# Kernel optimization log

Measured on AMD Instinct MI355X. Metric: run time of the kernel, lower is better.

Reference implementation:

```python
import jax, jax.numpy as jnp
import numpy as np

N_FQK, N_FV, N_REL, N_VAL, N_KNOW = 512, 256, 128, 64, 256
TOPK_QK, TOPK_V, TOPK_REL, TOPK_VAL = 64, 32, 16, 3
FQK_END = N_FQK
FV_END = N_FQK + N_FV
REL_END = FV_END + N_REL
VAL_END = REL_END + N_VAL
TOTAL = VAL_END + N_KNOW


def setup_inputs() -> dict:
    key = jax.random.key(0)
    k1, k2, k3, k4, k5 = jax.random.split(key, 5)
    B, S, D, DS = 8, 4096, 1024, 64
    x = jax.random.normal(k1, (B, S, D), dtype=jnp.float32)
    importance = jax.random.uniform(k2, (B, S), dtype=jnp.float32)
    proj_w = jax.random.normal(k3, (DS, D), dtype=jnp.float32) * (1.0 / np.sqrt(D))
    proj_b = jax.random.normal(k4, (DS,), dtype=jnp.float32) * 0.01
    neuron_emb = jax.random.normal(k5, (TOTAL, DS), dtype=jnp.float32) * 0.02
    return {"x": x, "importance": importance, "proj_w": proj_w,
            "proj_b": proj_b, "neuron_emb": neuron_emb}


def _topk_sparsify(w, k):
    # keep top-k values per row, zero elsewhere
    vals, idx = jax.lax.top_k(w, k)
    B = w.shape[0]
    sparse = jnp.zeros_like(w).at[jnp.arange(B)[:, None], idx].set(vals)
    return sparse, idx


def reference(x, importance, proj_w, proj_b, neuron_emb):
    # shared projection + normalized neuron embeddings (eval: dropout off,
    # no excitability bonus)
    h = jnp.einsum('bsd,kd->bsk', x, proj_w) + proj_b          # [B,S,d_space]
    emb_n = neuron_emb / jnp.linalg.norm(neuron_emb, axis=-1, keepdims=True)
    all_logits = jnp.einsum('bsk,nk->bsn', h, emb_n)            # [B,S,TOTAL]

    def agg(logits):
        pref = jax.nn.softmax(logits, axis=-1)                  # [B,S,n]
        return jnp.einsum('bs,bsn->bn', importance, pref)

    w_qk = agg(all_logits[..., :FQK_END])
    _, idx_qk = jax.lax.top_k(w_qk, TOPK_QK)
    idx_qk = jnp.sort(idx_qk, axis=-1)

    w_v = agg(all_logits[..., FQK_END:FV_END])
    _, idx_v = jax.lax.top_k(w_v, TOPK_V)
    idx_v = jnp.sort(idx_v, axis=-1)

    rel_logits = all_logits[..., FV_END:REL_END]
    # relational_Q and relational_K use the same logits slice (eval mode)
    rel_dense_Q = agg(rel_logits)
    rel_dense_K = agg(rel_logits)
    rel_Q, _ = _topk_sparsify(rel_dense_Q, TOPK_REL)
    rel_K, _ = _topk_sparsify(rel_dense_K, TOPK_REL)

    val_dense = agg(all_logits[..., REL_END:VAL_END])
    val_w, _ = _topk_sparsify(val_dense, TOPK_VAL)

    return idx_qk, idx_v, rel_Q, rel_K, val_w
```

## Files before the change

### kernel.cpp

```cpp
#include <hip/hip_runtime.h>


typedef short short8 __attribute__((ext_vector_type(8)));
typedef float f32x4 __attribute__((ext_vector_type(4)));
typedef unsigned int uint4v __attribute__((ext_vector_type(4)));

__device__ __forceinline__ unsigned short f32_to_bf16(float f) {
  unsigned u = __float_as_uint(f);
  u += 0x7FFF + ((u >> 16) & 1);
  return (unsigned short)(u >> 16);
}
__device__ __forceinline__ float bf16_to_f32(unsigned short h) {
  return __uint_as_float(((unsigned)h) << 16);
}

__device__ __forceinline__ unsigned cvt_pk_bf16(float a, float b) {
  unsigned r;
  asm("v_cvt_pk_bf16_f32 %0, %1, %2" : "=v"(r) : "v"(a), "v"(b));
  return r;
}

__device__ __forceinline__ void split8v(const f32x4& v0, const f32x4& v1,
                                        short8& hi, short8& lo) {
  unsigned hp[4], lp[4];
#pragma unroll
  for (int j = 0; j < 4; ++j) {
    float a = (j < 2) ? v0[2 * j] : v1[2 * j - 4];
    float b = (j < 2) ? v0[2 * j + 1] : v1[2 * j - 3];
    unsigned p = cvt_pk_bf16(a, b);
    float ra = a - __uint_as_float(p << 16);
    float rb = b - __uint_as_float(p & 0xFFFF0000u);
    hp[j] = p;
    lp[j] = cvt_pk_bf16(ra, rb);
  }
  hi = __builtin_bit_cast(short8, (uint4v){hp[0], hp[1], hp[2], hp[3]});
  lo = __builtin_bit_cast(short8, (uint4v){lp[0], lp[1], lp[2], lp[3]});
}

#define MFMA(a, b, c) __builtin_amdgcn_mfma_f32_16x16x32_bf16(a, b, c, 0, 0, 0)
#define WAITVM(n) asm volatile("s_waitcnt vmcnt(" #n ")" ::: "memory")

typedef const __attribute__((address_space(1))) unsigned int guint;
typedef __attribute__((address_space(3))) unsigned int luint;
__device__ __forceinline__ void stage16(const float* g, float* l) {
  __builtin_amdgcn_global_load_lds((guint*)g, (luint*)l, 16, 0, 0);
}
__device__ __forceinline__ void bar() {
  asm volatile("" ::: "memory");
  __builtin_amdgcn_s_barrier();
  asm volatile("" ::: "memory");
}

__global__ __launch_bounds__(256) void k_prep(const float* __restrict__ pw,
                                              const float* __restrict__ emb,
                                              unsigned short* __restrict__ whi,
                                              unsigned short* __restrict__ wlo,
                                              unsigned short* __restrict__ ehi,
                                              unsigned short* __restrict__ elo) {
  int tid = blockIdx.x * 256 + threadIdx.x;
  for (int i = tid; i < 65536; i += gridDim.x * 256) {
    float v = pw[i];
    unsigned short h = f32_to_bf16(v);
    whi[i] = h;
    wlo[i] = f32_to_bf16(v - bf16_to_f32(h));
  }
  int wid = tid >> 6, lane = tid & 63;
  int nw = gridDim.x * 4;
  for (int n = wid; n < 960; n += nw) {
    float v = emb[n * 64 + lane];
    float s = v * v;
#pragma unroll
    for (int off = 1; off < 64; off <<= 1) s += __shfl_xor(s, off);
    float vn = v / sqrtf(s);
    unsigned short h = f32_to_bf16(vn);
    ehi[n * 64 + lane] = h;
    elo[n * 64 + lane] = f32_to_bf16(vn - bf16_to_f32(h));
  }
}

__global__ __launch_bounds__(256, 4) void k_main(
    const float* __restrict__ x, const unsigned short* __restrict__ whi,
    const unsigned short* __restrict__ wlo, const float* __restrict__ pb,
    const unsigned short* __restrict__ ehi, const unsigned short* __restrict__ elo,
    const float* __restrict__ imp, float* __restrict__ pp) {
  __shared__ __align__(16) float xt[5][32][32];
  __shared__ __align__(16) unsigned short hxh[32][64];
  __shared__ __align__(16) unsigned short hxl[32][64];
  __shared__ float zpart[4][32][4];
  __shared__ float coefL[32][4];

  const int tid = threadIdx.x, w = tid >> 6, lane = tid & 63;
  const int q = lane >> 4, c = lane & 15;
  const int row0 = blockIdx.x * 32;
  const int nt0 = w;

  const int srow = tid >> 3;
  const int scol = ((tid & 7) ^ (srow & 7)) * 4;
  const float* sbase = x + (size_t)(row0 + srow) * 1024 + scol;
  auto STAGEX = [&](int slot, int ks) {
    stage16(sbase + ks * 32, &xt[slot][0][0] + (w << 8));
  };

  const unsigned short* bwh = whi + (size_t)(nt0 * 16 + c) * 1024 + q * 8;
  const unsigned short* bwl = wlo + (size_t)(nt0 * 16 + c) * 1024 + q * 8;

  f32x4 acc0 = {0.f, 0.f, 0.f, 0.f}, acc1 = {0.f, 0.f, 0.f, 0.f};

  const unsigned sw = (unsigned)((c & 7) << 4);
  const unsigned off1 = ((unsigned)(q * 32)) ^ sw;
  const unsigned off2 = ((unsigned)(q * 32 + 16)) ^ sw;
  const char* xby = (const char*)&xt[0][0][0] + (size_t)c * 128;

  int rs = 0, wsl = 4;
  auto projstep = [&](short8 B_hi, short8 B_lo) {
    const char* bp = xby + rs * 4096;
    f32x4 a0 = *(const f32x4*)(bp + off1);
    f32x4 a1 = *(const f32x4*)(bp + off2);
    f32x4 a2 = *(const f32x4*)(bp + 2048 + off1);
    f32x4 a3 = *(const f32x4*)(bp + 2048 + off2);
    short8 ah, al;
    split8v(a0, a1, ah, al);
    acc0 = MFMA(ah, B_hi, acc0);
    acc0 = MFMA(ah, B_lo, acc0);
    acc0 = MFMA(al, B_hi, acc0);
    split8v(a2, a3, ah, al);
    acc1 = MFMA(ah, B_hi, acc1);
    acc1 = MFMA(ah, B_lo, acc1);
    acc1 = MFMA(al, B_hi, acc1);
    ++rs; if (rs == 5) rs = 0;
  };
  auto loadB = [&](short8 (&h)[2], short8 (&l)[2], int g) {
    h[0] = *(const short8*)(bwh + (2 * g) * 32);
    h[1] = *(const short8*)(bwh + (2 * g + 1) * 32);
    l[0] = *(const short8*)(bwl + (2 * g) * 32);
    l[1] = *(const short8*)(bwl + (2 * g + 1) * 32);
  };

  short8 BhA[2], BlA[2], BhB[2], BlB[2];
  loadB(BhA, BlA, 0);
  STAGEX(0, 0); STAGEX(1, 1); STAGEX(2, 2); STAGEX(3, 3);

  auto gpair = [&](int g) {
    loadB(BhB, BlB, g + 1);
    WAITVM(6); bar();
    STAGEX(wsl, 2 * g + 4); ++wsl; if (wsl == 5) wsl = 0;
    projstep(BhA[0], BlA[0]);
    WAITVM(7); bar();
    STAGEX(wsl, 2 * g + 5); ++wsl; if (wsl == 5) wsl = 0;
    projstep(BhA[1], BlA[1]);
    loadB(BhA, BlA, g + 2);
    WAITVM(6); bar();
    STAGEX(wsl, 2 * g + 6); ++wsl; if (wsl == 5) wsl = 0;
    projstep(BhB[0], BlB[0]);
    WAITVM(7); bar();
    STAGEX(wsl, 2 * g + 7); ++wsl; if (wsl == 5) wsl = 0;
    projstep(BhB[1], BlB[1]);
  };
  gpair(0); gpair(2); gpair(4); gpair(6); gpair(8); gpair(10); gpair(12);
  loadB(BhB, BlB, 15);
  WAITVM(7); bar(); projstep(BhA[0], BlA[0]);
  WAITVM(6); bar(); projstep(BhA[1], BlA[1]);
  WAITVM(1); bar(); projstep(BhB[0], BlB[0]);
  WAITVM(0); bar(); projstep(BhB[1], BlB[1]);

  float bias = pb[nt0 * 16 + c];
#pragma unroll
  for (int mt = 0; mt < 2; ++mt) {
    f32x4 a = mt ? acc1 : acc0;
#pragma unroll
    for (int r = 0; r < 4; ++r) {
      float val = a[r] + bias;
      int row = mt * 16 + q * 4 + r;
      unsigned colb = (unsigned)((nt0 * 16 + c) * 2);
      unsigned o = (unsigned)(row * 128) + (colb ^ ((unsigned)(row & 7) << 4));
      unsigned short h = f32_to_bf16(val);
      *(unsigned short*)((char*)&hxh[0][0] + o) = h;
      *(unsigned short*)((char*)&hxl[0][0] + o) = f32_to_bf16(val - bf16_to_f32(h));
    }
  }
  __syncthreads();

  short8 Ahi[2][2], Alo[2][2];
#pragma unroll
  for (int mt = 0; mt < 2; ++mt) {
    int row = mt * 16 + c;
    unsigned rsw = (unsigned)((row & 7) << 4);
#pragma unroll
    for (int k2 = 0; k2 < 2; ++k2) {
      unsigned o = (unsigned)(row * 128) + (((unsigned)(k2 * 64 + q * 16)) ^ rsw);
      Ahi[mt][k2] = *(const short8*)((const char*)&hxh[0][0] + o);
      Alo[mt][k2] = *(const short8*)((const char*)&hxl[0][0] + o);
    }
  }

  const size_t ebq = (size_t)c * 64 + q * 8;
  short8 eA[4], eB[4];
  auto LOADE = [&](short8 (&d)[4], int i) {
    size_t eb = (size_t)(w + 4 * i) * 1024 + ebq;
    d[0] = *(const short8*)(ehi + eb);
    d[1] = *(const short8*)(ehi + eb + 32);
    d[2] = *(const short8*)(elo + eb);
    d[3] = *(const short8*)(elo + eb + 32);
  };

  f32x4 zacc0 = {0.f, 0.f, 0.f, 0.f}, zacc1 = {0.f, 0.f, 0.f, 0.f};
  auto zflush = [&](int seg) {
#pragma unroll
    for (int mt = 0; mt < 2; ++mt)
#pragma unroll
      for (int r = 0; r < 4; ++r) {
        float v = mt ? zacc1[r] : zacc0[r];
        v += __shfl_xor(v, 1); v += __shfl_xor(v, 2);
        v += __shfl_xor(v, 4); v += __shfl_xor(v, 8);
        if (c == 0) zpart[w][mt * 16 + q * 4 + r][seg] = v;
      }
    zacc0 = (f32x4){0.f, 0.f, 0.f, 0.f};
    zacc1 = (f32x4){0.f, 0.f, 0.f, 0.f};
  };

  int cur_seg = 0;
  auto step1 = [&](int i, short8 (&e)[4]) {
    int nt = w + 4 * i;
    int s = (nt < 32) ? 0 : (nt < 48) ? 1 : (nt < 56) ? 2 : 3;
    if (s != cur_seg) { zflush(cur_seg); cur_seg = s; }
#pragma unroll
    for (int mt = 0; mt < 2; ++mt) {
      f32x4 l = {0.f, 0.f, 0.f, 0.f};
      l = MFMA(Ahi[mt][0], e[0], l); l = MFMA(Ahi[mt][1], e[1], l);
      l = MFMA(Ahi[mt][0], e[2], l); l = MFMA(Ahi[mt][1], e[3], l);
      l = MFMA(Alo[mt][0], e[0], l); l = MFMA(Alo[mt][1], e[1], l);
#pragma unroll
      for (int r = 0; r < 4; ++r) {
        if (mt == 0) zacc0[r] += __expf(l[r]); else zacc1[r] += __expf(l[r]);
      }
    }
  };
  LOADE(eA, 0);
#pragma unroll
  for (int j = 0; j < 7; ++j) {
    LOADE(eB, 2 * j + 1); step1(2 * j, eA);
    LOADE(eA, 2 * j + 2); step1(2 * j + 1, eB);
  }
  step1(14, eA);
  zflush(cur_seg);
  __syncthreads();
  if (tid < 128) {
    int row = tid & 31, sg = tid >> 5;
    float Z = zpart[0][row][sg] + zpart[1][row][sg] + zpart[2][row][sg] + zpart[3][row][sg];
    coefL[row][sg] = imp[row0 + row] / Z;
  }
  __syncthreads();

  float* ppb = pp + (size_t)blockIdx.x * 960;
  f32x4 cf0, cf1;
  int cs2 = -1;
  auto step2 = [&](int i, short8 (&e)[4]) {
    int nt = w + 4 * i;
    int s = (nt < 32) ? 0 : (nt < 48) ? 1 : (nt < 56) ? 2 : 3;
    if (s != cs2) {
#pragma unroll
      for (int r = 0; r < 4; ++r) {
        cf0[r] = coefL[q * 4 + r][s];
        cf1[r] = coefL[16 + q * 4 + r][s];
      }
      cs2 = s;
    }
    float wsum = 0.f;
#pragma unroll
    for (int mt = 0; mt < 2; ++mt) {
      f32x4 l = {0.f, 0.f, 0.f, 0.f};
      l = MFMA(Ahi[mt][0], e[0], l); l = MFMA(Ahi[mt][1], e[1], l);
      l = MFMA(Ahi[mt][0], e[2], l); l = MFMA(Ahi[mt][1], e[3], l);
      l = MFMA(Alo[mt][0], e[0], l); l = MFMA(Alo[mt][1], e[1], l);
#pragma unroll
      for (int r = 0; r < 4; ++r)
        wsum = fmaf(__expf(l[r]), mt ? cf1[r] : cf0[r], wsum);
    }
    wsum += __shfl_xor(wsum, 16);
    wsum += __shfl_xor(wsum, 32);
    if (lane < 16) ppb[nt * 16 + c] = wsum;
  };
  LOADE(eA, 0);
#pragma unroll
  for (int j = 0; j < 7; ++j) {
    LOADE(eB, 2 * j + 1); step2(2 * j, eA);
    LOADE(eA, 2 * j + 2); step2(2 * j + 1, eB);
  }
  step2(14, eA);
}

__global__ __launch_bounds__(256) void k_topk(const float* __restrict__ pp,
                                              float* __restrict__ out) {
  __shared__ float vals[512];
  __shared__ int flags[512];
  int blk = blockIdx.x;
  int b = blk >> 2, t = blk & 3;
  int tid = threadIdx.x;
  const int Ns[4] = {512, 256, 128, 64};
  const int Ks[4] = {64, 32, 16, 3};
  const int Off[4] = {0, 512, 768, 896};
  int N = Ns[t], K = Ks[t], off = Off[t];
  for (int n = tid; n < N; n += 256) {
    const float* p = pp + (size_t)(b * 128) * 960 + off + n;
    float s0 = 0.f, s1 = 0.f, s2 = 0.f, s3 = 0.f;
    for (int rb = 0; rb < 128; rb += 4) {
      s0 += p[(size_t)(rb + 0) * 960];
      s1 += p[(size_t)(rb + 1) * 960];
      s2 += p[(size_t)(rb + 2) * 960];
      s3 += p[(size_t)(rb + 3) * 960];
    }
    vals[n] = (s0 + s1) + (s2 + s3);
  }
  __syncthreads();
  for (int n = tid; n < N; n += 256) {
    float v = vals[n];
    int rank = 0;
    for (int m = 0; m < N; ++m) {
      float u = vals[m];
      rank += (u > v || (u == v && m < n)) ? 1 : 0;
    }
    flags[n] = (rank < K) ? 1 : 0;
  }
  __syncthreads();
  if (t <= 1) {
    if (tid < 64) {
      int base = 0;
      for (int ch = 0; ch < N; ch += 64) {
        int n = ch + tid;
        int f = flags[n];
        unsigned long long mask = __ballot(f);
        if (f) {
          int pos = base + __popcll(mask & ((1ull << tid) - 1ull));
          if (t == 0) out[b * 64 + pos] = (float)n;
          else out[512 + b * 32 + pos] = (float)n;
        }
        base += __popcll(mask);
      }
    }
  } else if (t == 2) {
    for (int n = tid; n < 128; n += 256) {
      float v = flags[n] ? vals[n] : 0.f;
      out[768 + b * 128 + n] = v;
      out[1792 + b * 128 + n] = v;
    }
  } else {
    for (int n = tid; n < 64; n += 256) {
      float v = flags[n] ? vals[n] : 0.f;
      out[2816 + b * 64 + n] = v;
    }
  }
}

extern "C" void kernel_launch(void* const* d_in, const int* in_sizes, int n_in,
                              void* d_out, int out_size, void* d_ws, size_t ws_size,
                              hipStream_t stream) {
  const float* x   = (const float*)d_in[0];
  const float* imp = (const float*)d_in[1];
  const float* pw  = (const float*)d_in[2];
  const float* pb  = (const float*)d_in[3];
  const float* emb = (const float*)d_in[4];
  float* out = (float*)d_out;

  char* ws = (char*)d_ws;
  unsigned short* whi = (unsigned short*)(ws);
  unsigned short* wlo = (unsigned short*)(ws + 131072);
  unsigned short* ehi = (unsigned short*)(ws + 262144);
  unsigned short* elo = (unsigned short*)(ws + 385024);
  float*          pp  = (float*)(ws + 507904);

  hipLaunchKernelGGL(k_prep, dim3(64), dim3(256), 0, stream, pw, emb, whi, wlo, ehi, elo);
  hipLaunchKernelGGL(k_main, dim3(1024), dim3(256), 0, stream, x, whi, wlo, pb, ehi, elo, imp, pp);
  hipLaunchKernelGGL(k_topk, dim3(32), dim3(256), 0, stream, pp, out);
}
```

Baseline: 368.1 us.

## Stagger K-loop start per block and split logits MFMA chains

Each block now starts its K iteration at an offset derived from its block index, so concurrent blocks read different regions of the projection weights and x columns. The intent is to spread memory channel and cache traffic instead of having every block hit the same weight slice at once. The logits MFMA chain is split into two independent accumulators to shorten the dependency chain. The logits loops are also switched to unroll 1, likely to reduce code size and register pressure, at the cost of loop overhead and a less static segment selection.

```diff
diff --git a/kernel.cpp b/kernel.cpp
--- a/kernel.cpp
+++ b/kernel.cpp
@@ -93,12 +93,14 @@
   const int q = lane >> 4, c = lane & 15;
   const int row0 = blockIdx.x * 32;
   const int nt0 = w;
+  const int koff = blockIdx.x & 31;
 
   const int srow = tid >> 3;
   const int scol = ((tid & 7) ^ (srow & 7)) * 4;
   const float* sbase = x + (size_t)(row0 + srow) * 1024 + scol;
   auto STAGEX = [&](int slot, int ks) {
-    stage16(sbase + ks * 32, &xt[slot][0][0] + (w << 8));
+    int kp = (ks + koff) & 31;
+    stage16(sbase + kp * 32, &xt[slot][0][0] + (w << 8));
   };
 
   const unsigned short* bwh = whi + (size_t)(nt0 * 16 + c) * 1024 + q * 8;
@@ -130,10 +132,11 @@
     ++rs; if (rs == 5) rs = 0;
   };
   auto loadB = [&](short8 (&h)[2], short8 (&l)[2], int g) {
-    h[0] = *(const short8*)(bwh + (2 * g) * 32);
-    h[1] = *(const short8*)(bwh + (2 * g + 1) * 32);
-    l[0] = *(const short8*)(bwl + (2 * g) * 32);
-    l[1] = *(const short8*)(bwl + (2 * g + 1) * 32);
+    int k0 = (2 * g + koff) & 31, k1 = (2 * g + 1 + koff) & 31;
+    h[0] = *(const short8*)(bwh + k0 * 32);
+    h[1] = *(const short8*)(bwh + k1 * 32);
+    l[0] = *(const short8*)(bwl + k0 * 32);
+    l[1] = *(const short8*)(bwl + k1 * 32);
   };
 
   short8 BhA[2], BlA[2], BhB[2], BlB[2];
@@ -202,6 +205,13 @@
     d[2] = *(const short8*)(elo + eb);
     d[3] = *(const short8*)(elo + eb + 32);
   };
+  auto logits = [&](int mt, short8 (&e)[4]) -> f32x4 {
+    f32x4 la = {0.f, 0.f, 0.f, 0.f}, lb = {0.f, 0.f, 0.f, 0.f};
+    la = MFMA(Ahi[mt][0], e[0], la); la = MFMA(Ahi[mt][1], e[1], la);
+    lb = MFMA(Ahi[mt][0], e[2], lb); lb = MFMA(Ahi[mt][1], e[3], lb);
+    lb = MFMA(Alo[mt][0], e[0], lb); lb = MFMA(Alo[mt][1], e[1], lb);
+    return la + lb;
+  };
 
   f32x4 zacc0 = {0.f, 0.f, 0.f, 0.f}, zacc1 = {0.f, 0.f, 0.f, 0.f};
   auto zflush = [&](int seg) {
@@ -223,20 +233,15 @@
     int nt = w + 4 * i;
     int s = (nt < 32) ? 0 : (nt < 48) ? 1 : (nt < 56) ? 2 : 3;
     if (s != cur_seg) { zflush(cur_seg); cur_seg = s; }
-#pragma unroll
-    for (int mt = 0; mt < 2; ++mt) {
-      f32x4 l = {0.f, 0.f, 0.f, 0.f};
-      l = MFMA(Ahi[mt][0], e[0], l); l = MFMA(Ahi[mt][1], e[1], l);
-      l = MFMA(Ahi[mt][0], e[2], l); l = MFMA(Ahi[mt][1], e[3], l);
-      l = MFMA(Alo[mt][0], e[0], l); l = MFMA(Alo[mt][1], e[1], l);
-#pragma unroll
-      for (int r = 0; r < 4; ++r) {
-        if (mt == 0) zacc0[r] += __expf(l[r]); else zacc1[r] += __expf(l[r]);
-      }
+    f32x4 l0 = logits(0, e), l1 = logits(1, e);
+#pragma unroll
+    for (int r = 0; r < 4; ++r) {
+      zacc0[r] += __expf(l0[r]);
+      zacc1[r] += __expf(l1[r]);
     }
   };
   LOADE(eA, 0);
-#pragma unroll
+#pragma unroll 1
   for (int j = 0; j < 7; ++j) {
     LOADE(eB, 2 * j + 1); step1(2 * j, eA);
     LOADE(eA, 2 * j + 2); step1(2 * j + 1, eB);
@@ -265,23 +270,19 @@
       }
       cs2 = s;
     }
+    f32x4 l0 = logits(0, e), l1 = logits(1, e);
     float wsum = 0.f;
 #pragma unroll
-    for (int mt = 0; mt < 2; ++mt) {
-      f32x4 l = {0.f, 0.f, 0.f, 0.f};
-      l = MFMA(Ahi[mt][0], e[0], l); l = MFMA(Ahi[mt][1], e[1], l);
-      l = MFMA(Ahi[mt][0], e[2], l); l = MFMA(Ahi[mt][1], e[3], l);
-      l = MFMA(Alo[mt][0], e[0], l); l = MFMA(Alo[mt][1], e[1], l);
-#pragma unroll
-      for (int r = 0; r < 4; ++r)
-        wsum = fmaf(__expf(l[r]), mt ? cf1[r] : cf0[r], wsum);
+    for (int r = 0; r < 4; ++r) {
+      wsum = fmaf(__expf(l0[r]), cf0[r], wsum);
+      wsum = fmaf(__expf(l1[r]), cf1[r], wsum);
     }
     wsum += __shfl_xor(wsum, 16);
     wsum += __shfl_xor(wsum, 32);
     if (lane < 16) ppb[nt * 16 + c] = wsum;
   };
   LOADE(eA, 0);
-#pragma unroll
+#pragma unroll 1
   for (int j = 0; j < 7; ++j) {
     LOADE(eB, 2 * j + 1); step2(2 * j, eA);
     LOADE(eA, 2 * j + 2); step2(2 * j + 1, eB);
```

After: 326.4 us. 1.13x faster.
